# Kernel optimization log

Hardware: AMD Instinct MI355X
Metric: run time of the kernel (lower is better)

## Reference

```python
import jax, jax.numpy as jnp
import numpy as np

D_MODEL = 1024
EPS_DT = 1e-4
LN_EPS = 1e-5


def _layernorm(y, gamma, beta):
    mu = jnp.mean(y, axis=-1, keepdims=True)
    var = jnp.var(y, axis=-1, keepdims=True)
    return (y - mu) * jax.lax.rsqrt(var + LN_EPS) * gamma + beta


def setup_inputs() -> dict:
    key = jax.random.key(0)
    ks = jax.random.split(key, 8)
    B, T, D = 8, 4096, D_MODEL
    s = 1.0 / np.sqrt(D)  # ~ torch Linear default init scale
    return {
        "x": jax.random.normal(ks[0], (B, T, D), jnp.float32),
        "delta_t": jax.random.uniform(ks[1], (B, T, D), jnp.float32),
        "log_decay": jnp.zeros((D,), jnp.float32),
        "W_in": jax.random.uniform(ks[2], (D, D), jnp.float32, -s, s),
        "b_in": jax.random.uniform(ks[3], (D,), jnp.float32, -s, s),
        "W_gate": jax.random.uniform(ks[4], (D, D), jnp.float32, -s, s),
        "b_gate": jax.random.uniform(ks[5], (D,), jnp.float32, -s, s),
        "W_out": jax.random.uniform(ks[6], (D, D), jnp.float32, -s, s),
        "b_out": jax.random.uniform(ks[7], (D,), jnp.float32, -s, s),
        "gamma": jnp.ones((D,), jnp.float32),
        "beta": jnp.zeros((D,), jnp.float32),
    }


def reference(x, delta_t, log_decay, W_in, b_in, W_gate, b_gate, W_out, b_out, gamma, beta):
    B, T, D = x.shape
    decay = jax.nn.softplus(log_decay) + 1e-4          # [D]
    dt = jnp.maximum(delta_t, EPS_DT)                   # [B,T,D]
    lamb = jnp.exp(-decay * dt)                         # [B,T,D]
    # Drive terms depend only on x -> precompute in parallel (big GEMMs).
    update = jnp.einsum('btd,ed->bte', x, W_in) + b_in
    gate = jax.nn.sigmoid(jnp.einsum('btd,ed->bte', x, W_gate) + b_gate)
    drive = (1.0 - lamb) * gate * update                # [B,T,D]

    def step(state, inputs):
        l_t, d_t = inputs
        state = l_t * state + d_t
        return state, state

    state0 = jnp.zeros((B, D), x.dtype)
    final_state, states = jax.lax.scan(
        step, state0,
        (jnp.swapaxes(lamb, 0, 1), jnp.swapaxes(drive, 0, 1)))
    states = jnp.swapaxes(states, 0, 1)                 # [B,T,D]
    # dropout is identity in eval mode
    y = states + jnp.einsum('btd,ed->bte', states, W_out) + b_out
    out = _layernorm(y, gamma, beta)
    return out, final_state
```

## Files before the change

kernel.cpp:

```cpp
#include <hip/hip_runtime.h>
#include <hip/hip_bf16.h>

#define D_MODEL 1024
#define BATCH 8
#define SEQ 4096
#define MROWS (BATCH*SEQ)
#define NC 64
#define CL 64

typedef __attribute__((ext_vector_type(4))) float f32x4;
typedef __attribute__((ext_vector_type(8))) short s16x8;

__device__ __forceinline__ unsigned short f2bf(float f){
  union { float f; unsigned int u; } v; v.f = f;
  return (unsigned short)((v.u + 0x7fffu + ((v.u >> 16) & 1u)) >> 16);
}
__device__ __forceinline__ float bf2f(unsigned int bits){
  union { unsigned int u; float f; } v; v.u = bits << 16; return v.f;
}

__device__ __forceinline__ void gload16(const void* g, void* l){
  __builtin_amdgcn_global_load_lds(
      (const __attribute__((address_space(1))) unsigned int*)g,
      (__attribute__((address_space(3))) unsigned int*)l, 16, 0, 0);
}

__global__ __launch_bounds__(256)
void prep_x_kernel(const float* __restrict__ x, unsigned short* __restrict__ xb, int n4){
  int i = blockIdx.x*256 + threadIdx.x;
  int stride = gridDim.x*256;
  for (; i < n4; i += stride){
    float4 v = ((const float4*)x)[i];
    ushort4 o;
    o.x = f2bf(v.x); o.y = f2bf(v.y); o.z = f2bf(v.z); o.w = f2bf(v.w);
    ((ushort4*)xb)[i] = o;
  }
}

__global__ __launch_bounds__(256)
void prep_w_kernel(const float* __restrict__ Wi, const float* __restrict__ Wg,
                   const float* __restrict__ Wo, const float* __restrict__ ld,
                   unsigned short* __restrict__ Wib, unsigned short* __restrict__ Wgb,
                   unsigned short* __restrict__ Wob, float* __restrict__ decay){
  int i = blockIdx.x*256 + threadIdx.x;
  {
    float4 a = ((const float4*)Wi)[i]; ushort4 o;
    o.x=f2bf(a.x); o.y=f2bf(a.y); o.z=f2bf(a.z); o.w=f2bf(a.w); ((ushort4*)Wib)[i]=o;
    a = ((const float4*)Wg)[i];
    o.x=f2bf(a.x); o.y=f2bf(a.y); o.z=f2bf(a.z); o.w=f2bf(a.w); ((ushort4*)Wgb)[i]=o;
    a = ((const float4*)Wo)[i];
    o.x=f2bf(a.x); o.y=f2bf(a.y); o.z=f2bf(a.z); o.w=f2bf(a.w); ((ushort4*)Wob)[i]=o;
  }
  if (i < D_MODEL){
    float v = ld[i];
    float sp = fmaxf(v, 0.f) + log1pf(expf(-fabsf(v)));
    decay[i] = sp + 1e-4f;
  }
}

__global__ __launch_bounds__(256, 2)
void gemm_dual_kernel(const unsigned short* __restrict__ Xb,
                      const unsigned short* __restrict__ Wib,
                      const unsigned short* __restrict__ Wgb,
                      const float* __restrict__ b_in,
                      const float* __restrict__ b_gate,
                      const float* __restrict__ decay,
                      const float* __restrict__ delta,
                      unsigned int* __restrict__ pack)
{
  __shared__ unsigned short sA[128*64];
  __shared__ unsigned short sBi[128*64];
  __shared__ unsigned short sBg[128*64];
  const int tid  = threadIdx.x;
  const int lane = tid & 63;
  const int wave = tid >> 6;
  const int wr = wave >> 1, wc = wave & 1;
  const int bid = blockIdx.x;
  const int swz = ((bid & 7) << 8) | (bid >> 3);
  const int bcol = (swz & 7) * 128;
  const int brow = (swz >> 3) * 128;

  const f32x4 zero = {0.f,0.f,0.f,0.f};
  f32x4 accU[4][4], accG[4][4];
  #pragma unroll
  for (int a=0;a<4;a++)
    #pragma unroll
    for (int b=0;b<4;b++){ accU[a][b]=zero; accG[a][b]=zero; }

  for (int kt = 0; kt < D_MODEL/64; ++kt){
    __syncthreads();
    const size_t kbyte = (size_t)kt*128;
    #pragma unroll
    for (int i=0;i<4;i++){
      const int ob = i*256 + wave*64;
      const int o  = ob + lane;
      const int r  = o >> 3;
      const int cb = ((o & 7) ^ (r & 7)) * 16;
      gload16((const char*)Xb  + (size_t)(brow + r)*(D_MODEL*2) + kbyte + cb, (char*)sA  + (size_t)ob*16);
      gload16((const char*)Wib + (size_t)(bcol + r)*(D_MODEL*2) + kbyte + cb, (char*)sBi + (size_t)ob*16);
      gload16((const char*)Wgb + (size_t)(bcol + r)*(D_MODEL*2) + kbyte + cb, (char*)sBg + (size_t)ob*16);
    }
    __syncthreads();
    #pragma unroll
    for (int ks=0; ks<2; ++ks){
      s16x8 af[4], bi[4], bg[4];
      #pragma unroll
      for (int mi=0; mi<4; mi++){
        int row = wr*64 + mi*16 + (lane & 15);
        int chunk = (ks*4 + (lane>>4)) ^ (row & 7);
        af[mi] = *(const s16x8*)((const char*)sA + row*128 + chunk*16);
      }
      #pragma unroll
      for (int ni=0; ni<4; ni++){
        int n = wc*64 + ni*16 + (lane & 15);
        int chunk = (ks*4 + (lane>>4)) ^ (n & 7);
        bi[ni] = *(const s16x8*)((const char*)sBi + n*128 + chunk*16);
        bg[ni] = *(const s16x8*)((const char*)sBg + n*128 + chunk*16);
      }
      #pragma unroll
      for (int mi=0; mi<4; mi++)
        #pragma unroll
        for (int ni=0; ni<4; ni++){
          accU[mi][ni] = __builtin_amdgcn_mfma_f32_16x16x32_bf16(af[mi], bi[ni], accU[mi][ni], 0,0,0);
          accG[mi][ni] = __builtin_amdgcn_mfma_f32_16x16x32_bf16(af[mi], bg[ni], accG[mi][ni], 0,0,0);
        }
    }
  }
  #pragma unroll
  for (int ni=0; ni<4; ni++){
    const int col = bcol + wc*64 + ni*16 + (lane & 15);
    const float vb = b_in[col], vg = b_gate[col], dc = decay[col];
    #pragma unroll
    for (int mi=0; mi<4; mi++){
      #pragma unroll
      for (int q=0; q<4; q++){
        const int row = brow + wr*64 + mi*16 + ((lane>>4)*4) + q;
        const size_t idx = (size_t)row*D_MODEL + col;
        float u = accU[mi][ni][q] + vb;
        float z = accG[mi][ni][q] + vg;
        float g = 1.f/(1.f + __expf(-z));
        float dt = fmaxf(delta[idx], 1e-4f);
        float lam = __expf(-dc*dt);
        float omla = 1.f - lam;
        float drv = omla * g * u;
        pack[idx] = ((unsigned int)f2bf(drv) << 16) | (unsigned int)f2bf(omla);
      }
    }
  }
}

__global__ __launch_bounds__(256)
void scan_passA(const unsigned int* __restrict__ pack, float* __restrict__ cA, float* __restrict__ cB){
  const int d0 = (blockIdx.x*256 + threadIdx.x)*2;
  const int c = blockIdx.y, b = blockIdx.z;
  size_t base = ((size_t)b*SEQ + (size_t)c*CL)*D_MODEL + d0;
  float A0=1.f, A1=1.f, s0=0.f, s1=0.f;
  #pragma unroll 8
  for (int t=0;t<CL;t++){
    uint2 p = *(const uint2*)(pack + base + (size_t)t*D_MODEL);
    float om0 = bf2f(p.x & 0xffffu), dr0 = bf2f(p.x >> 16);
    float om1 = bf2f(p.y & 0xffffu), dr1 = bf2f(p.y >> 16);
    float l0 = 1.f - om0, l1 = 1.f - om1;
    A0 *= l0; A1 *= l1;
    s0 = fmaf(l0, s0, dr0);
    s1 = fmaf(l1, s1, dr1);
  }
  const size_t ci = ((size_t)b*NC + c)*D_MODEL + d0;
  *(float2*)(cA+ci) = make_float2(A0,A1);
  *(float2*)(cB+ci) = make_float2(s0,s1);
}

__global__ __launch_bounds__(256)
void scan_passB(const float* __restrict__ cA, const float* __restrict__ cB,
                float* __restrict__ cS, float* __restrict__ fstate){
  const int d0 = (blockIdx.x*256 + threadIdx.x)*2;
  const int b = blockIdx.y;
  float s0=0.f, s1=0.f;
  for (int c=0;c<NC;c++){
    const size_t ci = ((size_t)b*NC + c)*D_MODEL + d0;
    *(float2*)(cS+ci) = make_float2(s0,s1);
    float2 a  = *(const float2*)(cA+ci);
    float2 bb = *(const float2*)(cB+ci);
    s0 = fmaf(a.x, s0, bb.x);
    s1 = fmaf(a.y, s1, bb.y);
  }
  *(float2*)(fstate + (size_t)b*D_MODEL + d0) = make_float2(s0,s1);
}

__global__ __launch_bounds__(256)
void scan_passC(const unsigned int* __restrict__ pack, const float* __restrict__ cS,
                unsigned short* __restrict__ statesb){
  const int d0 = (blockIdx.x*256 + threadIdx.x)*2;
  const int c = blockIdx.y, b = blockIdx.z;
  float2 sv = *(const float2*)(cS + ((size_t)b*NC + c)*D_MODEL + d0);
  float s0 = sv.x, s1 = sv.y;
  size_t base = ((size_t)b*SEQ + (size_t)c*CL)*D_MODEL + d0;
  #pragma unroll 8
  for (int t=0;t<CL;t++){
    uint2 p = *(const uint2*)(pack + base + (size_t)t*D_MODEL);
    float om0 = bf2f(p.x & 0xffffu), dr0 = bf2f(p.x >> 16);
    float om1 = bf2f(p.y & 0xffffu), dr1 = bf2f(p.y >> 16);
    s0 = fmaf(-om0, s0, s0) + dr0;
    s1 = fmaf(-om1, s1, s1) + dr1;
    unsigned int w = ((unsigned int)f2bf(s1) << 16) | (unsigned int)f2bf(s0);
    *(unsigned int*)(statesb + base + (size_t)t*D_MODEL) = w;
  }
}

__global__ __launch_bounds__(256, 3)
void gemm_out_kernel(const unsigned short* __restrict__ Sb,
                     const unsigned short* __restrict__ Wob,
                     const float* __restrict__ b_out,
                     float* __restrict__ y)
{
  __shared__ unsigned short sA[128*64];
  __shared__ unsigned short sB[128*64];
  const int tid  = threadIdx.x;
  const int lane = tid & 63;
  const int wave = tid >> 6;
  const int wr = wave >> 1, wc = wave & 1;
  const int bid = blockIdx.x;
  const int swz = ((bid & 7) << 8) | (bid >> 3);
  const int bcol = (swz & 7) * 128;
  const int brow = (swz >> 3) * 128;

  const f32x4 zero = {0.f,0.f,0.f,0.f};
  f32x4 acc[4][4];
  #pragma unroll
  for (int a=0;a<4;a++)
    #pragma unroll
    for (int b=0;b<4;b++) acc[a][b]=zero;

  for (int kt = 0; kt < D_MODEL/64; ++kt){
    __syncthreads();
    const size_t kbyte = (size_t)kt*128;
    #pragma unroll
    for (int i=0;i<4;i++){
      const int ob = i*256 + wave*64;
      const int o  = ob + lane;
      const int r  = o >> 3;
      const int cb = ((o & 7) ^ (r & 7)) * 16;
      gload16((const char*)Sb  + (size_t)(brow + r)*(D_MODEL*2) + kbyte + cb, (char*)sA + (size_t)ob*16);
      gload16((const char*)Wob + (size_t)(bcol + r)*(D_MODEL*2) + kbyte + cb, (char*)sB + (size_t)ob*16);
    }
    __syncthreads();
    #pragma unroll
    for (int ks=0; ks<2; ++ks){
      s16x8 af[4], bf[4];
      #pragma unroll
      for (int mi=0; mi<4; mi++){
        int row = wr*64 + mi*16 + (lane & 15);
        int chunk = (ks*4 + (lane>>4)) ^ (row & 7);
        af[mi] = *(const s16x8*)((const char*)sA + row*128 + chunk*16);
      }
      #pragma unroll
      for (int ni=0; ni<4; ni++){
        int n = wc*64 + ni*16 + (lane & 15);
        int chunk = (ks*4 + (lane>>4)) ^ (n & 7);
        bf[ni] = *(const s16x8*)((const char*)sB + n*128 + chunk*16);
      }
      #pragma unroll
      for (int mi=0; mi<4; mi++)
        #pragma unroll
        for (int ni=0; ni<4; ni++)
          acc[mi][ni] = __builtin_amdgcn_mfma_f32_16x16x32_bf16(af[mi], bf[ni], acc[mi][ni], 0,0,0);
    }
  }
  #pragma unroll
  for (int ni=0; ni<4; ni++){
    const int col = bcol + wc*64 + ni*16 + (lane & 15);
    const float vb = b_out[col];
    #pragma unroll
    for (int mi=0; mi<4; mi++){
      #pragma unroll
      for (int q=0; q<4; q++){
        const int row = brow + wr*64 + mi*16 + ((lane>>4)*4) + q;
        const size_t idx = (size_t)row*D_MODEL + col;
        y[idx] = acc[mi][ni][q] + vb;
      }
    }
  }
}

__global__ __launch_bounds__(256)
void ln_kernel(const float* __restrict__ y, const unsigned short* __restrict__ statesb,
               const float* __restrict__ gamma, const float* __restrict__ beta,
               float* __restrict__ out)
{
  const int row = blockIdx.x;
  const int tid = threadIdx.x;
  float4 v = ((const float4*)(y + (size_t)row*D_MODEL))[tid];
  ushort4 sb = ((const ushort4*)(statesb + (size_t)row*D_MODEL))[tid];
  v.x += bf2f(sb.x); v.y += bf2f(sb.y); v.z += bf2f(sb.z); v.w += bf2f(sb.w);
  float s = v.x+v.y+v.z+v.w;
  float q = v.x*v.x + v.y*v.y + v.z*v.z + v.w*v.w;
  #pragma unroll
  for (int off=32; off>0; off>>=1){ s += __shfl_xor(s, off); q += __shfl_xor(q, off); }
  __shared__ float rs[4], rq[4];
  const int wave = tid>>6, lane = tid&63;
  if (lane==0){ rs[wave]=s; rq[wave]=q; }
  __syncthreads();
  float ts = rs[0]+rs[1]+rs[2]+rs[3];
  float tq = rq[0]+rq[1]+rq[2]+rq[3];
  float mu  = ts * (1.f/D_MODEL);
  float var = tq * (1.f/D_MODEL) - mu*mu;
  float inv = rsqrtf(var + 1e-5f);
  float4 g = ((const float4*)gamma)[tid];
  float4 b = ((const float4*)beta)[tid];
  float4 o;
  o.x = (v.x-mu)*inv*g.x + b.x;
  o.y = (v.y-mu)*inv*g.y + b.y;
  o.z = (v.z-mu)*inv*g.z + b.z;
  o.w = (v.w-mu)*inv*g.w + b.w;
  ((float4*)(out + (size_t)row*D_MODEL))[tid] = o;
}

extern "C" void kernel_launch(void* const* d_in, const int* in_sizes, int n_in,
                              void* d_out, int out_size, void* d_ws, size_t ws_size,
                              hipStream_t stream) {
  const float* x         = (const float*)d_in[0];
  const float* delta     = (const float*)d_in[1];
  const float* log_decay = (const float*)d_in[2];
  const float* W_in      = (const float*)d_in[3];
  const float* b_in      = (const float*)d_in[4];
  const float* W_gate    = (const float*)d_in[5];
  const float* b_gate    = (const float*)d_in[6];
  const float* W_out     = (const float*)d_in[7];
  const float* b_out     = (const float*)d_in[8];
  const float* gamma     = (const float*)d_in[9];
  const float* beta      = (const float*)d_in[10];

  char* w = (char*)d_ws;
  unsigned short* xb   = (unsigned short*)(w);
  unsigned short* Wib  = (unsigned short*)(w + 67108864);
  unsigned short* Wgb  = (unsigned short*)(w + 69206016);
  unsigned short* Wob  = (unsigned short*)(w + 71303168);
  float*          decay= (float*)        (w + 73400320);
  float*          cA   = (float*)        (w + 73404416);
  float*          cB   = (float*)        (w + 75501568);
  float*          cS   = (float*)        (w + 77598720);
  unsigned int*   pack = (unsigned int*) (w + 79695872);
  float*          ybuf = (float*)pack;
  unsigned short* statesb = xb;

  float* out    = (float*)d_out;
  float* fstate = out + (size_t)MROWS*D_MODEL;

  hipLaunchKernelGGL(prep_x_kernel, dim3(8192), dim3(256), 0, stream, x, xb, MROWS*D_MODEL/4);
  hipLaunchKernelGGL(prep_w_kernel, dim3(1024), dim3(256), 0, stream,
                     W_in, W_gate, W_out, log_decay, Wib, Wgb, Wob, decay);
  hipLaunchKernelGGL(gemm_dual_kernel, dim3(2048), dim3(256), 0, stream,
                     xb, Wib, Wgb, b_in, b_gate, decay, delta, pack);
  hipLaunchKernelGGL(scan_passA, dim3(2,NC,BATCH), dim3(256), 0, stream, pack, cA, cB);
  hipLaunchKernelGGL(scan_passB, dim3(2,BATCH), dim3(256), 0, stream, cA, cB, cS, fstate);
  hipLaunchKernelGGL(scan_passC, dim3(2,NC,BATCH), dim3(256), 0, stream, pack, cS, statesb);
  hipLaunchKernelGGL(gemm_out_kernel, dim3(2048), dim3(256), 0, stream, statesb, Wob, b_out, ybuf);
  hipLaunchKernelGGL(ln_kernel, dim3(MROWS), dim3(256), 0, stream, ybuf, statesb, gamma, beta, out);
}
```

Measured before the change: 425.0 us.

## Replace GEMMs with 256x256 double-buffered 8-wave pipelined GEMM template

Replaces the fused dual GEMM and the output GEMM with one templated 512-thread kernel that computes a 256x256 tile. It double-buffers LDS in half-tiles, interleaving global-to-LDS staging with MFMA phases, and uses explicit waitcnt, barriers and setprio. The dual GEMM is split into two passes: the first writes the bf16 update into the output buffer as scratch, and the second reads it back in its epilogue to build the packed drive and decay values. This trades fusion of the shared X reads for larger tiles and better latency hiding, at the cost of an extra round trip of the update tensor through memory.

```diff
diff --git a/kernel.cpp b/kernel.cpp
--- a/kernel.cpp
+++ b/kernel.cpp
@@ -7,6 +7,9 @@
 #define MROWS (BATCH*SEQ)
 #define NC 64
 #define CL 64
+#define BK 64
+#define NKT (D_MODEL/BK)
+#define HTE (128*64)
 
 typedef __attribute__((ext_vector_type(4))) float f32x4;
 typedef __attribute__((ext_vector_type(8))) short s16x8;
@@ -23,6 +26,19 @@
   __builtin_amdgcn_global_load_lds(
       (const __attribute__((address_space(1))) unsigned int*)g,
       (__attribute__((address_space(3))) unsigned int*)l, 16, 0, 0);
+}
+
+__device__ __forceinline__ void stage_half(const unsigned short* __restrict__ g, int row0,
+                                           unsigned short* lds, int kt, int wid, int lane){
+  #pragma unroll
+  for (int s=0;s<2;s++){
+    const int ob = s*512 + wid*64;
+    const int o  = ob + lane;
+    const int r  = o >> 3;
+    const int c  = ((o & 7) ^ (r & 7)) * 16;
+    gload16((const char*)g + (size_t)(row0 + r)*(D_MODEL*2) + (size_t)kt*128 + c,
+            (char*)lds + (size_t)ob*16);
+  }
 }
 
 __global__ __launch_bounds__(256)
@@ -58,92 +74,130 @@
   }
 }
 
-__global__ __launch_bounds__(256, 2)
-void gemm_dual_kernel(const unsigned short* __restrict__ Xb,
-                      const unsigned short* __restrict__ Wib,
-                      const unsigned short* __restrict__ Wgb,
-                      const float* __restrict__ b_in,
-                      const float* __restrict__ b_gate,
-                      const float* __restrict__ decay,
-                      const float* __restrict__ delta,
-                      unsigned int* __restrict__ pack)
+
+#define PHASE(d, q, SB_, SD, SH, KOFF, VM) do {                                   \
+  if ((q) == 0) {                                                                 \
+    _Pragma("unroll")                                                             \
+    for (int n=0;n<4;n++){                                                        \
+      const int rl = (wcn&1)*64 + n*16 + (lane&15);                               \
+      _Pragma("unroll")                                                           \
+      for (int ks=0;ks<2;ks++){                                                   \
+        const int ch = (ks*4 + (lane>>4)) ^ (rl&7);                               \
+        bf[n][ks] = *(const s16x8*)((const char*)&sB[d][wcn>>1][0] + rl*128 + ch*16); \
+      }                                                                           \
+    }                                                                             \
+  }                                                                               \
+  _Pragma("unroll")                                                               \
+  for (int mi=0;mi<2;mi++){                                                       \
+    const int rl = ((q)*2+mi)*16 + (lane&15);                                     \
+    _Pragma("unroll")                                                             \
+    for (int ks=0;ks<2;ks++){                                                     \
+      const int ch = (ks*4 + (lane>>4)) ^ (rl&7);                                 \
+      af[mi][ks] = *(const s16x8*)((const char*)&sA[d][wr][0] + rl*128 + ch*16);  \
+    }                                                                             \
+  }                                                                               \
+  { int skt = kt + (KOFF); if (skt > NKT-1) skt = NKT-1;                          \
+    if (SB_) stage_half(Bglob, bcol + (SH)*128, &sB[SD][SH][0], skt, wid, lane);  \
+    else     stage_half(Aglob, brow + (SH)*128, &sA[SD][SH][0], skt, wid, lane); }\
+  if (VM) asm volatile("s_waitcnt vmcnt(4)" ::: "memory");                        \
+  __builtin_amdgcn_s_barrier();                                                   \
+  asm volatile("s_waitcnt lgkmcnt(0)" ::: "memory");                              \
+  __builtin_amdgcn_sched_barrier(0);                                              \
+  __builtin_amdgcn_s_setprio(1);                                                  \
+  _Pragma("unroll")                                                               \
+  for (int ks=0;ks<2;ks++)                                                        \
+    _Pragma("unroll")                                                             \
+    for (int mi=0;mi<2;mi++)                                                      \
+      _Pragma("unroll")                                                           \
+      for (int n=0;n<4;n++)                                                       \
+        acc[(q)*2+mi][n] = __builtin_amdgcn_mfma_f32_16x16x32_bf16(               \
+            af[mi][ks], bf[n][ks], acc[(q)*2+mi][n], 0,0,0);                      \
+  __builtin_amdgcn_s_setprio(0);                                                  \
+  __builtin_amdgcn_s_barrier();                                                   \
+} while(0)
+
+template<int MODE>
+__global__ __launch_bounds__(512, 2)
+void gemm8_kernel(const unsigned short* __restrict__ Aglob,
+                  const unsigned short* __restrict__ Bglob,
+                  const float* __restrict__ bias,
+                  const float* __restrict__ decay,
+                  const float* __restrict__ delta,
+                  const unsigned short* __restrict__ ubr,
+                  unsigned short* __restrict__ ubw,
+                  unsigned int* __restrict__ pack,
+                  float* __restrict__ y)
 {
-  __shared__ unsigned short sA[128*64];
-  __shared__ unsigned short sBi[128*64];
-  __shared__ unsigned short sBg[128*64];
+  __shared__ unsigned short sA[2][2][HTE];
+  __shared__ unsigned short sB[2][2][HTE];
   const int tid  = threadIdx.x;
   const int lane = tid & 63;
-  const int wave = tid >> 6;
-  const int wr = wave >> 1, wc = wave & 1;
-  const int bid = blockIdx.x;
-  const int swz = ((bid & 7) << 8) | (bid >> 3);
-  const int bcol = (swz & 7) * 128;
-  const int brow = (swz >> 3) * 128;
+  const int wid  = tid >> 6;
+  const int wr   = wid >> 2;
+  const int wcn  = wid & 3;
+  const int bid  = blockIdx.x;
+  const int swz  = ((bid & 7) << 6) | (bid >> 3);
+  const int bcol = (swz & 3) * 256;
+  const int brow = (swz >> 2) * 256;
 
   const f32x4 zero = {0.f,0.f,0.f,0.f};
-  f32x4 accU[4][4], accG[4][4];
+  f32x4 acc[8][4];
   #pragma unroll
-  for (int a=0;a<4;a++)
+  for (int m=0;m<8;m++)
     #pragma unroll
-    for (int b=0;b<4;b++){ accU[a][b]=zero; accG[a][b]=zero; }
-
-  for (int kt = 0; kt < D_MODEL/64; ++kt){
-    __syncthreads();
-    const size_t kbyte = (size_t)kt*128;
+    for (int n=0;n<4;n++) acc[m][n]=zero;
+
+  stage_half(Bglob, bcol+0,   &sB[0][0][0], 0, wid, lane);
+  stage_half(Bglob, bcol+128, &sB[0][1][0], 0, wid, lane);
+  stage_half(Aglob, brow+0,   &sA[0][0][0], 0, wid, lane);
+  stage_half(Aglob, brow+128, &sA[0][1][0], 0, wid, lane);
+  stage_half(Bglob, bcol+0,   &sB[1][0][0], 1, wid, lane);
+  stage_half(Bglob, bcol+128, &sB[1][1][0], 1, wid, lane);
+  asm volatile("s_waitcnt vmcnt(4)" ::: "memory");
+  __builtin_amdgcn_s_barrier();
+
+  for (int it = 0; it < NKT/2; ++it){
+    const int kt = it*2;
+    s16x8 bf[4][2];
+    s16x8 af[2][2];
+    PHASE(0,0, 0,1,0, 1, 0);
+    PHASE(0,1, 0,1,1, 1, 0);
+    PHASE(0,2, 1,0,0, 2, 0);
+    PHASE(0,3, 1,0,1, 2, 1);
+    PHASE(1,0, 0,0,0, 2, 0);
+    PHASE(1,1, 0,0,1, 2, 0);
+    PHASE(1,2, 1,1,0, 3, 0);
+    PHASE(1,3, 1,1,1, 3, 1);
+  }
+
+  asm volatile("s_waitcnt vmcnt(0)" ::: "memory");
+
+  #pragma unroll
+  for (int n=0;n<4;n++){
+    const int col = bcol + wcn*64 + n*16 + (lane & 15);
+    const float vb = bias[col];
+    float dc = 0.f;
+    if constexpr (MODE==1) dc = decay[col];
     #pragma unroll
-    for (int i=0;i<4;i++){
-      const int ob = i*256 + wave*64;
-      const int o  = ob + lane;
-      const int r  = o >> 3;
-      const int cb = ((o & 7) ^ (r & 7)) * 16;
-      gload16((const char*)Xb  + (size_t)(brow + r)*(D_MODEL*2) + kbyte + cb, (char*)sA  + (size_t)ob*16);
-      gload16((const char*)Wib + (size_t)(bcol + r)*(D_MODEL*2) + kbyte + cb, (char*)sBi + (size_t)ob*16);
-      gload16((const char*)Wgb + (size_t)(bcol + r)*(D_MODEL*2) + kbyte + cb, (char*)sBg + (size_t)ob*16);
-    }
-    __syncthreads();
-    #pragma unroll
-    for (int ks=0; ks<2; ++ks){
-      s16x8 af[4], bi[4], bg[4];
+    for (int m=0;m<8;m++){
       #pragma unroll
-      for (int mi=0; mi<4; mi++){
-        int row = wr*64 + mi*16 + (lane & 15);
-        int chunk = (ks*4 + (lane>>4)) ^ (row & 7);
-        af[mi] = *(const s16x8*)((const char*)sA + row*128 + chunk*16);
-      }
-      #pragma unroll
-      for (int ni=0; ni<4; ni++){
-        int n = wc*64 + ni*16 + (lane & 15);
-        int chunk = (ks*4 + (lane>>4)) ^ (n & 7);
-        bi[ni] = *(const s16x8*)((const char*)sBi + n*128 + chunk*16);
-        bg[ni] = *(const s16x8*)((const char*)sBg + n*128 + chunk*16);
-      }
-      #pragma unroll
-      for (int mi=0; mi<4; mi++)
-        #pragma unroll
-        for (int ni=0; ni<4; ni++){
-          accU[mi][ni] = __builtin_amdgcn_mfma_f32_16x16x32_bf16(af[mi], bi[ni], accU[mi][ni], 0,0,0);
-          accG[mi][ni] = __builtin_amdgcn_mfma_f32_16x16x32_bf16(af[mi], bg[ni], accG[mi][ni], 0,0,0);
+      for (int j=0;j<4;j++){
+        const int row = brow + wr*128 + m*16 + ((lane>>4)*4) + j;
+        const size_t idx = (size_t)row*D_MODEL + col;
+        const float v = acc[m][n][j] + vb;
+        if constexpr (MODE==0){
+          ubw[idx] = f2bf(v);
+        } else if constexpr (MODE==1){
+          const float u = bf2f((unsigned int)ubr[idx]);
+          const float g = 1.f/(1.f + __expf(-v));
+          const float dt = fmaxf(delta[idx], 1e-4f);
+          const float lam = __expf(-dc*dt);
+          const float omla = 1.f - lam;
+          const float drv = omla * g * u;
+          pack[idx] = ((unsigned int)f2bf(drv) << 16) | (unsigned int)f2bf(omla);
+        } else {
+          y[idx] = v;
         }
-    }
-  }
-  #pragma unroll
-  for (int ni=0; ni<4; ni++){
-    const int col = bcol + wc*64 + ni*16 + (lane & 15);
-    const float vb = b_in[col], vg = b_gate[col], dc = decay[col];
-    #pragma unroll
-    for (int mi=0; mi<4; mi++){
-      #pragma unroll
-      for (int q=0; q<4; q++){
-        const int row = brow + wr*64 + mi*16 + ((lane>>4)*4) + q;
-        const size_t idx = (size_t)row*D_MODEL + col;
-        float u = accU[mi][ni][q] + vb;
-        float z = accG[mi][ni][q] + vg;
-        float g = 1.f/(1.f + __expf(-z));
-        float dt = fmaxf(delta[idx], 1e-4f);
-        float lam = __expf(-dc*dt);
-        float omla = 1.f - lam;
-        float drv = omla * g * u;
-        pack[idx] = ((unsigned int)f2bf(drv) << 16) | (unsigned int)f2bf(omla);
       }
     }
   }
@@ -204,81 +258,6 @@
     s1 = fmaf(-om1, s1, s1) + dr1;
     unsigned int w = ((unsigned int)f2bf(s1) << 16) | (unsigned int)f2bf(s0);
     *(unsigned int*)(statesb + base + (size_t)t*D_MODEL) = w;
-  }
-}
-
-__global__ __launch_bounds__(256, 3)
-void gemm_out_kernel(const unsigned short* __restrict__ Sb,
-                     const unsigned short* __restrict__ Wob,
-                     const float* __restrict__ b_out,
-                     float* __restrict__ y)
-{
-  __shared__ unsigned short sA[128*64];
-  __shared__ unsigned short sB[128*64];
-  const int tid  = threadIdx.x;
-  const int lane = tid & 63;
-  const int wave = tid >> 6;
-  const int wr = wave >> 1, wc = wave & 1;
-  const int bid = blockIdx.x;
-  const int swz = ((bid & 7) << 8) | (bid >> 3);
-  const int bcol = (swz & 7) * 128;
-  const int brow = (swz >> 3) * 128;
-
-  const f32x4 zero = {0.f,0.f,0.f,0.f};
-  f32x4 acc[4][4];
-  #pragma unroll
-  for (int a=0;a<4;a++)
-    #pragma unroll
-    for (int b=0;b<4;b++) acc[a][b]=zero;
-
-  for (int kt = 0; kt < D_MODEL/64; ++kt){
-    __syncthreads();
-    const size_t kbyte = (size_t)kt*128;
-    #pragma unroll
-    for (int i=0;i<4;i++){
-      const int ob = i*256 + wave*64;
-      const int o  = ob + lane;
-      const int r  = o >> 3;
-      const int cb = ((o & 7) ^ (r & 7)) * 16;
-      gload16((const char*)Sb  + (size_t)(brow + r)*(D_MODEL*2) + kbyte + cb, (char*)sA + (size_t)ob*16);
-      gload16((const char*)Wob + (size_t)(bcol + r)*(D_MODEL*2) + kbyte + cb, (char*)sB + (size_t)ob*16);
-    }
-    __syncthreads();
-    #pragma unroll
-    for (int ks=0; ks<2; ++ks){
-      s16x8 af[4], bf[4];
-      #pragma unroll
-      for (int mi=0; mi<4; mi++){
-        int row = wr*64 + mi*16 + (lane & 15);
-        int chunk = (ks*4 + (lane>>4)) ^ (row & 7);
-        af[mi] = *(const s16x8*)((const char*)sA + row*128 + chunk*16);
-      }
-      #pragma unroll
-      for (int ni=0; ni<4; ni++){
-        int n = wc*64 + ni*16 + (lane & 15);
-        int chunk = (ks*4 + (lane>>4)) ^ (n & 7);
-        bf[ni] = *(const s16x8*)((const char*)sB + n*128 + chunk*16);
-      }
-      #pragma unroll
-      for (int mi=0; mi<4; mi++)
-        #pragma unroll
-        for (int ni=0; ni<4; ni++)
-          acc[mi][ni] = __builtin_amdgcn_mfma_f32_16x16x32_bf16(af[mi], bf[ni], acc[mi][ni], 0,0,0);
-    }
-  }
-  #pragma unroll
-  for (int ni=0; ni<4; ni++){
-    const int col = bcol + wc*64 + ni*16 + (lane & 15);
-    const float vb = b_out[col];
-    #pragma unroll
-    for (int mi=0; mi<4; mi++){
-      #pragma unroll
-      for (int q=0; q<4; q++){
-        const int row = brow + wr*64 + mi*16 + ((lane>>4)*4) + q;
-        const size_t idx = (size_t)row*D_MODEL + col;
-        y[idx] = acc[mi][ni][q] + vb;
-      }
-    }
   }
 }
 
@@ -345,15 +324,19 @@
 
   float* out    = (float*)d_out;
   float* fstate = out + (size_t)MROWS*D_MODEL;
+  unsigned short* ub = (unsigned short*)d_out;
 
   hipLaunchKernelGGL(prep_x_kernel, dim3(8192), dim3(256), 0, stream, x, xb, MROWS*D_MODEL/4);
   hipLaunchKernelGGL(prep_w_kernel, dim3(1024), dim3(256), 0, stream,
                      W_in, W_gate, W_out, log_decay, Wib, Wgb, Wob, decay);
-  hipLaunchKernelGGL(gemm_dual_kernel, dim3(2048), dim3(256), 0, stream,
-                     xb, Wib, Wgb, b_in, b_gate, decay, delta, pack);
+  gemm8_kernel<0><<<dim3(512), dim3(512), 0, stream>>>(
+      xb, Wib, b_in, nullptr, nullptr, nullptr, ub, nullptr, nullptr);
+  gemm8_kernel<1><<<dim3(512), dim3(512), 0, stream>>>(
+      xb, Wgb, b_gate, decay, delta, ub, nullptr, pack, nullptr);
   hipLaunchKernelGGL(scan_passA, dim3(2,NC,BATCH), dim3(256), 0, stream, pack, cA, cB);
   hipLaunchKernelGGL(scan_passB, dim3(2,BATCH), dim3(256), 0, stream, cA, cB, cS, fstate);
   hipLaunchKernelGGL(scan_passC, dim3(2,NC,BATCH), dim3(256), 0, stream, pack, cS, statesb);
-  hipLaunchKernelGGL(gemm_out_kernel, dim3(2048), dim3(256), 0, stream, statesb, Wob, b_out, ybuf);
+  gemm8_kernel<2><<<dim3(512), dim3(512), 0, stream>>>(
+      statesb, Wob, b_out, nullptr, nullptr, nullptr, nullptr, nullptr, ybuf);
   hipLaunchKernelGGL(ln_kernel, dim3(MROWS), dim3(256), 0, stream, ybuf, statesb, gamma, beta, out);
 }
```

New measurement: 684.6 us. 1.61x slower.

## Load GEMM weight fragments directly from global memory and store GEMM output in bf16

Applied to the files above, without the earlier changes.

Both GEMM kernels stop staging the weight (B) tiles in LDS and instead read the bf16 MFMA fragments straight from global memory per k-step, keeping only the activation tile in shared memory. This cuts LDS use, which could raise occupancy, and removes the LDS traffic for weights. The cost is uncoalesced 16-byte global loads of weight rows that rely on L2 hits, with no prefetch. Separately, the output GEMM now writes y as bf16 instead of fp32, roughly halving that intermediate's write and read traffic at some loss of precision before the layernorm.

```diff
diff --git a/kernel.cpp b/kernel.cpp
--- a/kernel.cpp
+++ b/kernel.cpp
@@ -69,8 +69,6 @@
                       unsigned int* __restrict__ pack)
 {
   __shared__ unsigned short sA[128*64];
-  __shared__ unsigned short sBi[128*64];
-  __shared__ unsigned short sBg[128*64];
   const int tid  = threadIdx.x;
   const int lane = tid & 63;
   const int wave = tid >> 6;
@@ -87,35 +85,41 @@
     #pragma unroll
     for (int b=0;b<4;b++){ accU[a][b]=zero; accG[a][b]=zero; }
 
+  const int kfrag = (lane>>4)*8;
+
   for (int kt = 0; kt < D_MODEL/64; ++kt){
     __syncthreads();
-    const size_t kbyte = (size_t)kt*128;
+    #pragma unroll
+    for (int i=0;i<4;i++){
+      const int ob = i*64 + wave*16 + (i==0?0:0) ;
+      (void)ob;
+    }
     #pragma unroll
     for (int i=0;i<4;i++){
       const int ob = i*256 + wave*64;
       const int o  = ob + lane;
       const int r  = o >> 3;
-      const int cb = ((o & 7) ^ (r & 7)) * 16;
-      gload16((const char*)Xb  + (size_t)(brow + r)*(D_MODEL*2) + kbyte + cb, (char*)sA  + (size_t)ob*16);
-      gload16((const char*)Wib + (size_t)(bcol + r)*(D_MODEL*2) + kbyte + cb, (char*)sBi + (size_t)ob*16);
-      gload16((const char*)Wgb + (size_t)(bcol + r)*(D_MODEL*2) + kbyte + cb, (char*)sBg + (size_t)ob*16);
+      const int c  = ((o & 7) ^ (r & 7)) * 16;
+      gload16((const char*)Xb + (size_t)(brow + r)*(D_MODEL*2) + (size_t)kt*128 + c,
+              (char*)sA + (size_t)ob*16);
     }
     __syncthreads();
     #pragma unroll
     for (int ks=0; ks<2; ++ks){
-      s16x8 af[4], bi[4], bg[4];
+      s16x8 bi[4], bg[4], af[4];
+      #pragma unroll
+      for (int ni=0; ni<4; ni++){
+        const int col = bcol + wc*64 + ni*16 + (lane & 15);
+        const unsigned short* bp = Wib + (size_t)col*D_MODEL + kt*64 + ks*32 + kfrag;
+        const unsigned short* gp = Wgb + (size_t)col*D_MODEL + kt*64 + ks*32 + kfrag;
+        bi[ni] = *(const s16x8*)bp;
+        bg[ni] = *(const s16x8*)gp;
+      }
       #pragma unroll
       for (int mi=0; mi<4; mi++){
-        int row = wr*64 + mi*16 + (lane & 15);
-        int chunk = (ks*4 + (lane>>4)) ^ (row & 7);
+        const int row = wr*64 + mi*16 + (lane & 15);
+        const int chunk = (ks*4 + (lane>>4)) ^ (row & 7);
         af[mi] = *(const s16x8*)((const char*)sA + row*128 + chunk*16);
-      }
-      #pragma unroll
-      for (int ni=0; ni<4; ni++){
-        int n = wc*64 + ni*16 + (lane & 15);
-        int chunk = (ks*4 + (lane>>4)) ^ (n & 7);
-        bi[ni] = *(const s16x8*)((const char*)sBi + n*128 + chunk*16);
-        bg[ni] = *(const s16x8*)((const char*)sBg + n*128 + chunk*16);
       }
       #pragma unroll
       for (int mi=0; mi<4; mi++)
@@ -211,10 +215,9 @@
 void gemm_out_kernel(const unsigned short* __restrict__ Sb,
                      const unsigned short* __restrict__ Wob,
                      const float* __restrict__ b_out,
-                     float* __restrict__ y)
+                     unsigned short* __restrict__ yb)
 {
   __shared__ unsigned short sA[128*64];
-  __shared__ unsigned short sB[128*64];
   const int tid  = threadIdx.x;
   const int lane = tid & 63;
   const int wave = tid >> 6;
@@ -231,33 +234,33 @@
     #pragma unroll
     for (int b=0;b<4;b++) acc[a][b]=zero;
 
+  const int kfrag = (lane>>4)*8;
+
   for (int kt = 0; kt < D_MODEL/64; ++kt){
     __syncthreads();
-    const size_t kbyte = (size_t)kt*128;
     #pragma unroll
     for (int i=0;i<4;i++){
       const int ob = i*256 + wave*64;
       const int o  = ob + lane;
       const int r  = o >> 3;
-      const int cb = ((o & 7) ^ (r & 7)) * 16;
-      gload16((const char*)Sb  + (size_t)(brow + r)*(D_MODEL*2) + kbyte + cb, (char*)sA + (size_t)ob*16);
-      gload16((const char*)Wob + (size_t)(bcol + r)*(D_MODEL*2) + kbyte + cb, (char*)sB + (size_t)ob*16);
+      const int c  = ((o & 7) ^ (r & 7)) * 16;
+      gload16((const char*)Sb + (size_t)(brow + r)*(D_MODEL*2) + (size_t)kt*128 + c,
+              (char*)sA + (size_t)ob*16);
     }
     __syncthreads();
     #pragma unroll
     for (int ks=0; ks<2; ++ks){
-      s16x8 af[4], bf[4];
+      s16x8 bf[4], af[4];
+      #pragma unroll
+      for (int ni=0; ni<4; ni++){
+        const int col = bcol + wc*64 + ni*16 + (lane & 15);
+        bf[ni] = *(const s16x8*)(Wob + (size_t)col*D_MODEL + kt*64 + ks*32 + kfrag);
+      }
       #pragma unroll
       for (int mi=0; mi<4; mi++){
-        int row = wr*64 + mi*16 + (lane & 15);
-        int chunk = (ks*4 + (lane>>4)) ^ (row & 7);
+        const int row = wr*64 + mi*16 + (lane & 15);
+        const int chunk = (ks*4 + (lane>>4)) ^ (row & 7);
         af[mi] = *(const s16x8*)((const char*)sA + row*128 + chunk*16);
-      }
-      #pragma unroll
-      for (int ni=0; ni<4; ni++){
-        int n = wc*64 + ni*16 + (lane & 15);
-        int chunk = (ks*4 + (lane>>4)) ^ (n & 7);
-        bf[ni] = *(const s16x8*)((const char*)sB + n*128 + chunk*16);
       }
       #pragma unroll
       for (int mi=0; mi<4; mi++)
@@ -276,22 +279,26 @@
       for (int q=0; q<4; q++){
         const int row = brow + wr*64 + mi*16 + ((lane>>4)*4) + q;
         const size_t idx = (size_t)row*D_MODEL + col;
-        y[idx] = acc[mi][ni][q] + vb;
-      }
-    }
-  }
-}
-
-__global__ __launch_bounds__(256)
-void ln_kernel(const float* __restrict__ y, const unsigned short* __restrict__ statesb,
+        yb[idx] = f2bf(acc[mi][ni][q] + vb);
+      }
+    }
+  }
+}
+
+__global__ __launch_bounds__(256)
+void ln_kernel(const unsigned short* __restrict__ yb, const unsigned short* __restrict__ statesb,
                const float* __restrict__ gamma, const float* __restrict__ beta,
                float* __restrict__ out)
 {
   const int row = blockIdx.x;
   const int tid = threadIdx.x;
-  float4 v = ((const float4*)(y + (size_t)row*D_MODEL))[tid];
+  ushort4 yv = ((const ushort4*)(yb + (size_t)row*D_MODEL))[tid];
   ushort4 sb = ((const ushort4*)(statesb + (size_t)row*D_MODEL))[tid];
-  v.x += bf2f(sb.x); v.y += bf2f(sb.y); v.z += bf2f(sb.z); v.w += bf2f(sb.w);
+  float4 v;
+  v.x = bf2f(yv.x) + bf2f(sb.x);
+  v.y = bf2f(yv.y) + bf2f(sb.y);
+  v.z = bf2f(yv.z) + bf2f(sb.z);
+  v.w = bf2f(yv.w) + bf2f(sb.w);
   float s = v.x+v.y+v.z+v.w;
   float q = v.x*v.x + v.y*v.y + v.z*v.z + v.w*v.w;
   #pragma unroll
@@ -340,7 +347,7 @@
   float*          cB   = (float*)        (w + 75501568);
   float*          cS   = (float*)        (w + 77598720);
   unsigned int*   pack = (unsigned int*) (w + 79695872);
-  float*          ybuf = (float*)pack;
+  unsigned short* ybuf = (unsigned short*)pack;
   unsigned short* statesb = xb;
 
   float* out    = (float*)d_out;
```

New measurement: 588.7 us. +38.5%, slower.
